# Optimization experiments

Measured on AMD Instinct MI355X. Metric: run time of the kernel, lower is better.

The kernel has to match this reference:

```python
import jax, jax.numpy as jnp
import numpy as np

ALPHA = 0.2  # LeakyReLU negative slope


def setup_inputs() -> dict:
    key = jax.random.key(0)
    k0, k1, k2, k3 = jax.random.split(key, 4)
    N, E, C_IN, H, C_PH = 50000, 800000, 128, 4, 32  # per-head dim = out_channels // num_heads
    node_feats = jax.random.normal(k0, (N, C_IN), dtype=jnp.float32)
    edge_index = jax.random.randint(k1, (2, E), 0, N, dtype=jnp.int64)
    # Linear(in_channels, num_heads * per_head): W is [H*C_PH, C_IN], b is [H*C_PH]
    W = jax.random.normal(k2, (H * C_PH, C_IN), dtype=jnp.float32) * 0.1
    b = jnp.zeros((H * C_PH,), dtype=jnp.float32)
    # attention vector a: [H, 2*C_PH]
    a = jax.random.normal(k3, (H, 2 * C_PH), dtype=jnp.float32) * 0.1
    return {"node_feats": node_feats, "edge_index": edge_index, "W": W, "b": b, "a": a}


def reference(node_feats, edge_index, W, b, a):
    H, twoC = a.shape
    C = twoC // 2
    N = node_feats.shape[0]
    # Linear projection, then split heads: [N, H, C]
    h = (node_feats @ W.T + b).reshape(N, H, C)
    # logits[e,h] = <h[src_e] ++ h[dst_e], a[h]> ; split the dot product so we
    # compute per-node partial scores once and gather scalars per edge.
    s_src = jnp.einsum('nhc,hc->nh', h, a[:, :C])   # [N, H]
    s_dst = jnp.einsum('nhc,hc->nh', h, a[:, C:])   # [N, H]
    logits = s_src[edge_index[0]] + s_dst[edge_index[1]]  # [E, H]
    logits = jax.nn.leaky_relu(logits, negative_slope=ALPHA)
    # Original applies softmax over dim=-2, i.e. across ALL edges per head.
    return jax.nn.softmax(logits, axis=0)
```

## Files before the change

### kernel.cpp

```cpp
#include <hip/hip_runtime.h>

#define ALPHA 0.2f

#define WS_SUM   0
#define NSLOT    16
#define WS_S     1024

__global__ __launch_bounds__(256) void k_proj(const float* __restrict__ x,
                                              const float* __restrict__ W,
                                              const float* __restrict__ b,
                                              const float* __restrict__ a,
                                              float* __restrict__ ws, int N) {
    __shared__ float lw[1152];
    __shared__ float lb[8];
    int t = threadIdx.x;
    #pragma unroll
    for (int j = 0; j < 4; ++j) {
        int idx = t + 256 * j;
        int k = idx & 127;
        int h = (idx >> 7) & 3;
        int dstf = idx >> 9;
        const float* Wp = W + (size_t)(h * 32) * 128 + k;
        const float* ap = a + h * 64 + dstf * 32;
        float acc = 0.f;
        #pragma unroll
        for (int c = 0; c < 32; ++c)
            acc = fmaf(Wp[(size_t)c * 128], ap[c], acc);
        lw[dstf * 576 + h * 144 + k + 4 * (k >> 5)] = acc;
    }
    if (t < 8) {
        int h = t & 3, dstf = t >> 2;
        float acc = 0.f;
        #pragma unroll
        for (int c = 0; c < 32; ++c)
            acc = fmaf(b[h * 32 + c], a[h * 64 + dstf * 32 + c], acc);
        lb[t] = acc;
    }
    if (blockIdx.x == 0 && t < 64) ws[WS_SUM + t * 16] = 0.f;
    __syncthreads();

    int q = t & 3;
    int node = blockIdx.x * 64 + (t >> 2);
    float aS0=0,aS1=0,aS2=0,aS3=0,aD0=0,aD1=0,aD2=0,aD3=0;
    if (node < N) {
        const float4* xp = (const float4*)(x + (size_t)node * 128 + q * 32);
        int wb = q * 36;
        #pragma unroll
        for (int i = 0; i < 8; ++i) {
            float4 xv = xp[i];
            int o = wb + i * 4;
            float4 w;
            w = *(const float4*)&lw[o];          aS0 += xv.x*w.x + xv.y*w.y + xv.z*w.z + xv.w*w.w;
            w = *(const float4*)&lw[144 + o];    aS1 += xv.x*w.x + xv.y*w.y + xv.z*w.z + xv.w*w.w;
            w = *(const float4*)&lw[288 + o];    aS2 += xv.x*w.x + xv.y*w.y + xv.z*w.z + xv.w*w.w;
            w = *(const float4*)&lw[432 + o];    aS3 += xv.x*w.x + xv.y*w.y + xv.z*w.z + xv.w*w.w;
            w = *(const float4*)&lw[576 + o];    aD0 += xv.x*w.x + xv.y*w.y + xv.z*w.z + xv.w*w.w;
            w = *(const float4*)&lw[720 + o];    aD1 += xv.x*w.x + xv.y*w.y + xv.z*w.z + xv.w*w.w;
            w = *(const float4*)&lw[864 + o];    aD2 += xv.x*w.x + xv.y*w.y + xv.z*w.z + xv.w*w.w;
            w = *(const float4*)&lw[1008 + o];   aD3 += xv.x*w.x + xv.y*w.y + xv.z*w.z + xv.w*w.w;
        }
    }
    aS0 += __shfl_xor(aS0, 1); aS0 += __shfl_xor(aS0, 2);
    aS1 += __shfl_xor(aS1, 1); aS1 += __shfl_xor(aS1, 2);
    aS2 += __shfl_xor(aS2, 1); aS2 += __shfl_xor(aS2, 2);
    aS3 += __shfl_xor(aS3, 1); aS3 += __shfl_xor(aS3, 2);
    aD0 += __shfl_xor(aD0, 1); aD0 += __shfl_xor(aD0, 2);
    aD1 += __shfl_xor(aD1, 1); aD1 += __shfl_xor(aD1, 2);
    aD2 += __shfl_xor(aD2, 1); aD2 += __shfl_xor(aD2, 2);
    aD3 += __shfl_xor(aD3, 1); aD3 += __shfl_xor(aD3, 2);
    if (q == 0 && node < N) {
        float4* sp = (float4*)(ws + WS_S + (size_t)node * 8);
        sp[0] = make_float4(aS0 + lb[0], aS1 + lb[1], aS2 + lb[2], aS3 + lb[3]);
        sp[1] = make_float4(aD0 + lb[4], aD1 + lb[5], aD2 + lb[6], aD3 + lb[7]);
    }
}

__device__ __forceinline__ float leaky_exp(float z) {
    z = (z >= 0.f) ? z : ALPHA * z;
    return __expf(z);
}

__global__ __launch_bounds__(256) void k_edge_sum(const int* __restrict__ ei,
                                                  const float* __restrict__ s,
                                                  float* __restrict__ sums, int E) {
    int tid = blockIdx.x * blockDim.x + threadIdx.x;
    int T = gridDim.x * blockDim.x;
    float l0 = 0.f, l1 = 0.f, l2 = 0.f, l3 = 0.f;
    for (int e = tid; e < E; e += T) {
        int src = ei[e];
        int dst = ei[E + e];
        float4 ss = *(const float4*)(s + (size_t)src * 8);
        float4 sd = *(const float4*)(s + (size_t)dst * 8 + 4);
        l0 += leaky_exp(ss.x + sd.x);
        l1 += leaky_exp(ss.y + sd.y);
        l2 += leaky_exp(ss.z + sd.z);
        l3 += leaky_exp(ss.w + sd.w);
    }
    #pragma unroll
    for (int m = 1; m < 64; m <<= 1) {
        l0 += __shfl_xor(l0, m);
        l1 += __shfl_xor(l1, m);
        l2 += __shfl_xor(l2, m);
        l3 += __shfl_xor(l3, m);
    }
    __shared__ float red[4][4];
    int wv = threadIdx.x >> 6;
    if ((threadIdx.x & 63) == 0) {
        red[wv][0] = l0; red[wv][1] = l1; red[wv][2] = l2; red[wv][3] = l3;
    }
    __syncthreads();
    if (threadIdx.x < 4) {
        int h = threadIdx.x;
        int slot = blockIdx.x & (NSLOT - 1);
        atomicAdd(&sums[(h * NSLOT + slot) * 16],
                  red[0][h] + red[1][h] + red[2][h] + red[3][h]);
    }
}

__global__ __launch_bounds__(256) void k_finish(const int* __restrict__ ei,
                                                const float* __restrict__ s,
                                                const float* __restrict__ sums,
                                                float* __restrict__ out, int E) {
    __shared__ float inv[4];
    if (threadIdx.x < 4) {
        int h = threadIdx.x;
        float acc = 0.f;
        #pragma unroll
        for (int j = 0; j < NSLOT; ++j) acc += sums[(h * NSLOT + j) * 16];
        inv[h] = 1.0f / acc;
    }
    __syncthreads();
    int tid = blockIdx.x * blockDim.x + threadIdx.x;
    int T = gridDim.x * blockDim.x;
    for (int e = tid; e < E; e += T) {
        int src = ei[e];
        int dst = ei[E + e];
        float4 ss = *(const float4*)(s + (size_t)src * 8);
        float4 sd = *(const float4*)(s + (size_t)dst * 8 + 4);
        float4 v;
        v.x = leaky_exp(ss.x + sd.x) * inv[0];
        v.y = leaky_exp(ss.y + sd.y) * inv[1];
        v.z = leaky_exp(ss.z + sd.z) * inv[2];
        v.w = leaky_exp(ss.w + sd.w) * inv[3];
        *(float4*)(out + (size_t)e * 4) = v;
    }
}

extern "C" void kernel_launch(void* const* d_in, const int* in_sizes, int n_in,
                              void* d_out, int out_size, void* d_ws, size_t ws_size,
                              hipStream_t stream) {
    const float* x  = (const float*)d_in[0];
    const int*   ei = (const int*)d_in[1];
    const float* W  = (const float*)d_in[2];
    const float* b  = (const float*)d_in[3];
    const float* a  = (const float*)d_in[4];
    float* out = (float*)d_out;
    float* ws  = (float*)d_ws;

    const int CIN = 128;
    int N = in_sizes[0] / CIN;
    int E = in_sizes[1] / 2;

    k_proj<<<(N + 63) / 64, 256, 0, stream>>>(x, W, b, a, ws, N);
    k_edge_sum<<<1024, 256, 0, stream>>>(ei, ws + WS_S, ws + WS_SUM, E);
    k_finish<<<1024, 256, 0, stream>>>(ei, ws + WS_S, ws + WS_SUM, out, E);
}
```

Baseline: 110.4 us.

## Fuse edge-sum and normalize kernels with a grid-wide atomic barrier

Merges the two edge passes into one persistent kernel. Each thread keeps its up to four exp values in registers, the blocks meet at a software grid barrier built on an atomic counter, and then each thread scales and writes its values. This removes the second gather of edge indices and node scores and one kernel launch. In exchange it relies on all 1024 blocks being resident at once; otherwise the barrier deadlocks. It also only covers E ≤ 4·grid·256 edges, which holds here (800k ≤ ~1.05M).

```diff
diff --git a/kernel.cpp b/kernel.cpp
--- a/kernel.cpp
+++ b/kernel.cpp
@@ -1,10 +1,10 @@
 #include <hip/hip_runtime.h>
 
 #define ALPHA 0.2f
+#define NSLOT 16
 
-#define WS_SUM   0
-#define NSLOT    16
-#define WS_S     1024
+#define WS_CNT 1024
+#define WS_S   1040
 
 __global__ __launch_bounds__(256) void k_proj(const float* __restrict__ x,
                                               const float* __restrict__ W,
@@ -36,7 +36,10 @@
             acc = fmaf(b[h * 32 + c], a[h * 64 + dstf * 32 + c], acc);
         lb[t] = acc;
     }
-    if (blockIdx.x == 0 && t < 64) ws[WS_SUM + t * 16] = 0.f;
+    if (blockIdx.x == 0) {
+        if (t < 64) ws[t * 16] = 0.f;
+        if (t == 64) *(int*)(ws + WS_CNT) = 0;
+    }
     __syncthreads();
 
     int q = t & 3;
@@ -80,21 +83,31 @@
     return __expf(z);
 }
 
-__global__ __launch_bounds__(256) void k_edge_sum(const int* __restrict__ ei,
-                                                  const float* __restrict__ s,
-                                                  float* __restrict__ sums, int E) {
+__global__ __launch_bounds__(256, 4) void k_edge_fused(const int* __restrict__ ei,
+                                                       float* __restrict__ ws,
+                                                       float* __restrict__ out, int E) {
+    const float* s = ws + WS_S;
     int tid = blockIdx.x * blockDim.x + threadIdx.x;
     int T = gridDim.x * blockDim.x;
+
+    float4 v[4];
     float l0 = 0.f, l1 = 0.f, l2 = 0.f, l3 = 0.f;
-    for (int e = tid; e < E; e += T) {
-        int src = ei[e];
-        int dst = ei[E + e];
-        float4 ss = *(const float4*)(s + (size_t)src * 8);
-        float4 sd = *(const float4*)(s + (size_t)dst * 8 + 4);
-        l0 += leaky_exp(ss.x + sd.x);
-        l1 += leaky_exp(ss.y + sd.y);
-        l2 += leaky_exp(ss.z + sd.z);
-        l3 += leaky_exp(ss.w + sd.w);
+    #pragma unroll
+    for (int i = 0; i < 4; ++i) {
+        int e = tid + i * T;
+        if (e < E) {
+            int src = ei[e];
+            int dst = ei[E + e];
+            float4 ss = *(const float4*)(s + (size_t)src * 8);
+            float4 sd = *(const float4*)(s + (size_t)dst * 8 + 4);
+            float4 r;
+            r.x = leaky_exp(ss.x + sd.x);
+            r.y = leaky_exp(ss.y + sd.y);
+            r.z = leaky_exp(ss.z + sd.z);
+            r.w = leaky_exp(ss.w + sd.w);
+            v[i] = r;
+            l0 += r.x; l1 += r.y; l2 += r.z; l3 += r.w;
+        }
     }
     #pragma unroll
     for (int m = 1; m < 64; m <<= 1) {
@@ -112,37 +125,45 @@
     if (threadIdx.x < 4) {
         int h = threadIdx.x;
         int slot = blockIdx.x & (NSLOT - 1);
-        atomicAdd(&sums[(h * NSLOT + slot) * 16],
+        atomicAdd(&ws[(h * NSLOT + slot) * 16],
                   red[0][h] + red[1][h] + red[2][h] + red[3][h]);
     }
-}
 
-__global__ __launch_bounds__(256) void k_finish(const int* __restrict__ ei,
-                                                const float* __restrict__ s,
-                                                const float* __restrict__ sums,
-                                                float* __restrict__ out, int E) {
+    __syncthreads();
+    int* cnt = (int*)(ws + WS_CNT);
+    if (threadIdx.x == 0) {
+        __threadfence();
+        atomicAdd(cnt, 1);
+        while (__hip_atomic_load(cnt, __ATOMIC_ACQUIRE, __HIP_MEMORY_SCOPE_AGENT)
+               < (int)gridDim.x) {
+            __builtin_amdgcn_s_sleep(1);
+        }
+    }
+    __syncthreads();
+
+    __shared__ float sred[64];
     __shared__ float inv[4];
+    if (threadIdx.x < 64)
+        sred[threadIdx.x] = __hip_atomic_load(&ws[threadIdx.x * 16],
+                                              __ATOMIC_RELAXED, __HIP_MEMORY_SCOPE_AGENT);
+    __syncthreads();
     if (threadIdx.x < 4) {
-        int h = threadIdx.x;
         float acc = 0.f;
         #pragma unroll
-        for (int j = 0; j < NSLOT; ++j) acc += sums[(h * NSLOT + j) * 16];
-        inv[h] = 1.0f / acc;
+        for (int j = 0; j < NSLOT; ++j) acc += sred[threadIdx.x * NSLOT + j];
+        inv[threadIdx.x] = 1.0f / acc;
     }
     __syncthreads();
-    int tid = blockIdx.x * blockDim.x + threadIdx.x;
-    int T = gridDim.x * blockDim.x;
-    for (int e = tid; e < E; e += T) {
-        int src = ei[e];
-        int dst = ei[E + e];
-        float4 ss = *(const float4*)(s + (size_t)src * 8);
-        float4 sd = *(const float4*)(s + (size_t)dst * 8 + 4);
-        float4 v;
-        v.x = leaky_exp(ss.x + sd.x) * inv[0];
-        v.y = leaky_exp(ss.y + sd.y) * inv[1];
-        v.z = leaky_exp(ss.z + sd.z) * inv[2];
-        v.w = leaky_exp(ss.w + sd.w) * inv[3];
-        *(float4*)(out + (size_t)e * 4) = v;
+    float ix = inv[0], iy = inv[1], iz = inv[2], iw = inv[3];
+
+    #pragma unroll
+    for (int i = 0; i < 4; ++i) {
+        int e = tid + i * T;
+        if (e < E) {
+            float4 r = v[i];
+            r.x *= ix; r.y *= iy; r.z *= iz; r.w *= iw;
+            *(float4*)(out + (size_t)e * 4) = r;
+        }
     }
 }
 
@@ -162,6 +183,5 @@
     int E = in_sizes[1] / 2;
 
     k_proj<<<(N + 63) / 64, 256, 0, stream>>>(x, W, b, a, ws, N);
-    k_edge_sum<<<1024, 256, 0, stream>>>(ei, ws + WS_S, ws + WS_SUM, E);
-    k_finish<<<1024, 256, 0, stream>>>(ei, ws + WS_S, ws + WS_SUM, out, E);
+    k_edge_fused<<<1024, 256, 0, stream>>>(ei, ws, out, E);
 }
```

New measurement: 223.9 us. 2.03x slower.
